# Performance work log

Hardware: AMD Instinct MI355X
Metric: run time of the kernel (lower is better)

Reference implementation:

```python
import jax, jax.numpy as jnp
import numpy as np


def setup_inputs() -> dict:
    key = jax.random.key(0)
    k1, k2 = jax.random.split(key)
    N, K, D = 32768, 1024, 512
    x = jax.random.normal(k1, (N, D), dtype=jnp.float32)
    centers = jax.random.normal(k2, (K, D), dtype=jnp.float32)
    return {"x": x, "centers": centers}


def reference(x, centers):
    # broadcasted (x[:,None]-c[None])**2 sum without the O(N*K*D) intermediate)
    x_sq = jnp.sum(x * x, axis=-1, keepdims=True)           # [N, 1]
    c_sq = jnp.sum(centers * centers, axis=-1)              # [K]
    cross = jnp.einsum('nd,kd->nk', x, centers)             # [N, K]
    norm_squared = x_sq + c_sq[None, :] - 2.0 * cross       # [N, K]
    # exp(-d/2) / sum_k exp(-d/2) == softmax(-d/2) over clusters
    probabilities = jax.nn.softmax(-0.5 * norm_squared, axis=1)
    return probabilities
```

## Files before the change

kernel.cpp:

```cpp
#include <hip/hip_runtime.h>
#include <stdint.h>


namespace {
constexpr int N_ROWS  = 32768;
constexpr int K_CL    = 1024;
constexpr int D_DIM   = 512;
constexpr int BM      = 64;
constexpr int THREADS = 512;
constexpr int WAVES   = 8;
constexpr int NSLICE  = 16;
}

typedef __bf16 bf16_t;
typedef __bf16 bf16x8 __attribute__((ext_vector_type(8)));
typedef __bf16 bf16x4 __attribute__((ext_vector_type(4)));
typedef float  f32x4  __attribute__((ext_vector_type(4)));

__global__ __launch_bounds__(64) void prep_kernel(const float* __restrict__ centers,
                                                  bf16_t* __restrict__ bpack,
                                                  float* __restrict__ bias) {
  const int col = blockIdx.x, lane = threadIdx.x;
  const int t = lane >> 2, g = lane & 3;
  const float* src = centers + (size_t)col * D_DIM + lane * 8;
  bf16x8 hi, lo;
  float ssq = 0.f;
  #pragma unroll
  for (int i = 0; i < 8; ++i) {
    float v = src[i];
    ssq += v * v;
    bf16_t h = (bf16_t)v;
    hi[i] = h;
    lo[i] = (bf16_t)(v - (float)h);
  }
  const int jh = col >> 9, c = col & 511;
  *(bf16x8*)(bpack + ((size_t)(4 * t + jh)     * 2048 + g * 512 + c) * 8) = hi;
  *(bf16x8*)(bpack + ((size_t)(4 * t + 2 + jh) * 2048 + g * 512 + c) * 8) = lo;
  for (int off = 32; off; off >>= 1) ssq += __shfl_down(ssq, off, 64);
  if (lane == 0) bias[col] = -0.5f * ssq;
}

__global__ __launch_bounds__(THREADS, 2) void cluster_kernel(
    const float* __restrict__ x, const bf16_t* __restrict__ bpack,
    const float* __restrict__ bias, float* __restrict__ out) {
  __shared__ bf16_t Abuf[2][2][2048];
  __shared__ float  red[WAVES * BM];
  __shared__ float  fin[BM];

  const int tid  = threadIdx.x;
  const int wid  = tid >> 6;
  const int lane = tid & 63;
  const int g    = lane >> 4;
  const int l15  = lane & 15;
  const int brow = blockIdx.x * BM;
  const int xrow = tid >> 3, q = tid & 7, gk = q >> 1, qh = q & 1;

  float bcol[8];
  #pragma unroll
  for (int cc = 0; cc < 8; ++cc)
    bcol[cc] = bias[(cc >> 2) * 512 + wid * 64 + (cc & 3) * 16 + l15];

  f32x4 acc[4][8];
  #pragma unroll
  for (int rb = 0; rb < 4; ++rb)
    #pragma unroll
    for (int cc = 0; cc < 8; ++cc) acc[rb][cc] = (f32x4){0.f, 0.f, 0.f, 0.f};

  const bf16x8* bbase =
      (const bf16x8*)bpack + ((size_t)g * 512 + wid * 64 + l15);

#define LOADB(S, DST)                                                          \
  {                                                                            \
    const bf16x8* p_ = bbase + (size_t)(S) * 2048;                             \
    _Pragma("unroll")                                                          \
    for (int cb_ = 0; cb_ < 4; ++cb_) (DST)[cb_] = p_[cb_ * 16];               \
  }
#define CONVERT(XV, PAR)                                                       \
  {                                                                            \
    bf16x4 h4_, l4_;                                                           \
    float vv_[4] = {(XV).x, (XV).y, (XV).z, (XV).w};                           \
    _Pragma("unroll")                                                          \
    for (int i_ = 0; i_ < 4; ++i_) {                                           \
      bf16_t h_ = (bf16_t)vv_[i_];                                             \
      h4_[i_] = h_;                                                            \
      l4_[i_] = (bf16_t)(vv_[i_] - (float)h_);                                 \
    }                                                                          \
    *(bf16x4*)&Abuf[(PAR)][0][(gk * 64 + xrow) * 8 + qh * 4] = h4_;            \
    *(bf16x4*)&Abuf[(PAR)][1][(gk * 64 + xrow) * 8 + qh * 4] = l4_;            \
  }
#define COMPUTE(BREG, HALF, WITH_LO)                                           \
  {                                                                            \
    _Pragma("unroll")                                                          \
    for (int cb = 0; cb < 4; ++cb) {                                           \
      _Pragma("unroll")                                                        \
      for (int rb = 0; rb < 4; ++rb)                                           \
        acc[rb][(HALF) * 4 + cb] = __builtin_amdgcn_mfma_f32_16x16x32_bf16(    \
            ahi[rb], (BREG)[cb], acc[rb][(HALF) * 4 + cb], 0, 0, 0);           \
      if (WITH_LO) {                                                           \
        _Pragma("unroll")                                                      \
        for (int rb = 0; rb < 4; ++rb)                                         \
          acc[rb][(HALF) * 4 + cb] = __builtin_amdgcn_mfma_f32_16x16x32_bf16(  \
              alo[rb], (BREG)[cb], acc[rb][(HALF) * 4 + cb], 0, 0, 0);         \
      }                                                                        \
    }                                                                          \
  }

  const float* xbase = x + (size_t)(brow + xrow) * D_DIM + q * 4;
  bf16x8 bcur[4], bnxt[4];

  {
    float4 xv0 = *(const float4*)xbase;
    CONVERT(xv0, 0)
    LOADB(0, bcur)
  }
  __syncthreads();

  bf16x8 ahi[4], alo[4];

  #pragma unroll 1
  for (int t = 0; t < NSLICE; ++t) {
    const int s0 = 4 * t;

    #pragma unroll
    for (int rb = 0; rb < 4; ++rb) {
      ahi[rb] = *(const bf16x8*)&Abuf[t & 1][0][(g * 64 + rb * 16 + l15) * 8];
      alo[rb] = *(const bf16x8*)&Abuf[t & 1][1][(g * 64 + rb * 16 + l15) * 8];
    }

    LOADB(s0 + 1, bnxt)
    COMPUTE(bcur, 0, 1)

    LOADB(s0 + 2, bcur)
    float4 xv = *(const float4*)(xbase + ((t + 1) & 15) * 32);
    COMPUTE(bnxt, 1, 1)

    LOADB(s0 + 3, bnxt)
    CONVERT(xv, (t + 1) & 1)
    COMPUTE(bcur, 0, 0)

    LOADB((s0 + 4) & 63, bcur)
    COMPUTE(bnxt, 1, 0)

    __syncthreads();
  }

  float rmax[4][4];
  #pragma unroll
  for (int rb = 0; rb < 4; ++rb) {
    #pragma unroll
    for (int j = 0; j < 4; ++j) {
      float m = -3.0e38f;
      #pragma unroll
      for (int cc = 0; cc < 8; ++cc) {
        float v = acc[rb][cc][j] + bcol[cc];
        acc[rb][cc][j] = v;
        m = fmaxf(m, v);
      }
      m = fmaxf(m, __shfl_xor(m, 1, 64));
      m = fmaxf(m, __shfl_xor(m, 2, 64));
      m = fmaxf(m, __shfl_xor(m, 4, 64));
      m = fmaxf(m, __shfl_xor(m, 8, 64));
      rmax[rb][j] = m;
    }
  }
  if (l15 == 0) {
    #pragma unroll
    for (int rb = 0; rb < 4; ++rb)
      #pragma unroll
      for (int j = 0; j < 4; ++j)
        red[wid * BM + rb * 16 + g * 4 + j] = rmax[rb][j];
  }
  __syncthreads();
  if (tid < BM) {
    float m = red[tid];
    #pragma unroll
    for (int w = 1; w < WAVES; ++w) m = fmaxf(m, red[w * BM + tid]);
    fin[tid] = m;
  }
  __syncthreads();

  #pragma unroll
  for (int rb = 0; rb < 4; ++rb) {
    #pragma unroll
    for (int j = 0; j < 4; ++j) {
      float m = fin[rb * 16 + g * 4 + j];
      float s = 0.f;
      #pragma unroll
      for (int cc = 0; cc < 8; ++cc) {
        float e = __expf(acc[rb][cc][j] - m);
        acc[rb][cc][j] = e;
        s += e;
      }
      s += __shfl_xor(s, 1, 64);
      s += __shfl_xor(s, 2, 64);
      s += __shfl_xor(s, 4, 64);
      s += __shfl_xor(s, 8, 64);
      rmax[rb][j] = s;
    }
  }
  __syncthreads();
  if (l15 == 0) {
    #pragma unroll
    for (int rb = 0; rb < 4; ++rb)
      #pragma unroll
      for (int j = 0; j < 4; ++j)
        red[wid * BM + rb * 16 + g * 4 + j] = rmax[rb][j];
  }
  __syncthreads();
  if (tid < BM) {
    float s = 0.f;
    #pragma unroll
    for (int w = 0; w < WAVES; ++w) s += red[w * BM + tid];
    fin[tid] = 1.0f / s;
  }
  __syncthreads();

  #pragma unroll
  for (int rb = 0; rb < 4; ++rb) {
    #pragma unroll
    for (int j = 0; j < 4; ++j) {
      const int row = rb * 16 + g * 4 + j;
      const float rs = fin[row];
      #pragma unroll
      for (int cc = 0; cc < 8; ++cc) {
        const int col = (cc >> 2) * 512 + wid * 64 + (cc & 3) * 16 + l15;
        out[(size_t)(brow + row) * K_CL + col] = acc[rb][cc][j] * rs;
      }
    }
  }
}

extern "C" void kernel_launch(void* const* d_in, const int* in_sizes, int n_in,
                              void* d_out, int out_size, void* d_ws, size_t ws_size,
                              hipStream_t stream) {
  const float* x       = (const float*)d_in[0];
  const float* centers = (const float*)d_in[1];
  float* out = (float*)d_out;

  bf16_t* bpack = (bf16_t*)d_ws;
  float*  bias  = (float*)((char*)d_ws + (size_t)64 * 32768);

  prep_kernel<<<K_CL, 64, 0, stream>>>(centers, bpack, bias);
  cluster_kernel<<<N_ROWS / BM, THREADS, 0, stream>>>(x, bpack, bias, out);
}
```

Baseline: 109.5 us.

## Stage B fragments through a 4-deep async global-to-LDS ring buffer

```diff
diff --git a/kernel.cpp b/kernel.cpp
--- a/kernel.cpp
+++ b/kernel.cpp
@@ -17,6 +17,12 @@
 typedef __bf16 bf16x4 __attribute__((ext_vector_type(4)));
 typedef float  f32x4  __attribute__((ext_vector_type(4)));
 
+__device__ inline void async_copy16(const void* g, void* l) {
+  __builtin_amdgcn_global_load_lds(
+      (const __attribute__((address_space(1))) uint32_t*)g,
+      (__attribute__((address_space(3))) uint32_t*)l, 16, 0, 0);
+}
+
 __global__ __launch_bounds__(64) void prep_kernel(const float* __restrict__ centers,
                                                   bf16_t* __restrict__ bpack,
                                                   float* __restrict__ bias) {
@@ -43,6 +49,7 @@
 __global__ __launch_bounds__(THREADS, 2) void cluster_kernel(
     const float* __restrict__ x, const bf16_t* __restrict__ bpack,
     const float* __restrict__ bias, float* __restrict__ out) {
+  __shared__ bf16_t Bbuf[4][16384];
   __shared__ bf16_t Abuf[2][2][2048];
   __shared__ float  red[WAVES * BM];
   __shared__ float  fin[BM];
@@ -55,25 +62,20 @@
   const int brow = blockIdx.x * BM;
   const int xrow = tid >> 3, q = tid & 7, gk = q >> 1, qh = q & 1;
 
-  float bcol[8];
-  #pragma unroll
-  for (int cc = 0; cc < 8; ++cc)
-    bcol[cc] = bias[(cc >> 2) * 512 + wid * 64 + (cc & 3) * 16 + l15];
-
   f32x4 acc[4][8];
   #pragma unroll
   for (int rb = 0; rb < 4; ++rb)
     #pragma unroll
     for (int cc = 0; cc < 8; ++cc) acc[rb][cc] = (f32x4){0.f, 0.f, 0.f, 0.f};
 
-  const bf16x8* bbase =
-      (const bf16x8*)bpack + ((size_t)g * 512 + wid * 64 + l15);
-
-#define LOADB(S, DST)                                                          \
+#define STAGE_B(S)                                                             \
   {                                                                            \
-    const bf16x8* p_ = bbase + (size_t)(S) * 2048;                             \
-    _Pragma("unroll")                                                          \
-    for (int cb_ = 0; cb_ < 4; ++cb_) (DST)[cb_] = p_[cb_ * 16];               \
+    const char* gs_ = (const char*)bpack + (size_t)((S) & 63) * 32768 +        \
+                      wid * 4096 + lane * 16;                                  \
+    char* ld_ = (char*)&Bbuf[(S) & 3][0] + wid * 4096;                         \
+    _Pragma("unroll")                                                          \
+    for (int i_ = 0; i_ < 4; ++i_)                                             \
+      async_copy16(gs_ + i_ * 1024, ld_ + i_ * 1024);                          \
   }
 #define CONVERT(XV, PAR)                                                       \
   {                                                                            \
@@ -88,32 +90,45 @@
     *(bf16x4*)&Abuf[(PAR)][0][(gk * 64 + xrow) * 8 + qh * 4] = h4_;            \
     *(bf16x4*)&Abuf[(PAR)][1][(gk * 64 + xrow) * 8 + qh * 4] = l4_;            \
   }
-#define COMPUTE(BREG, HALF, WITH_LO)                                           \
+#define COMPUTE(BUF, HALF, WITH_LO)                                            \
   {                                                                            \
+    const bf16_t* bb = &Bbuf[(BUF)][0];                                        \
+    bf16x8 bfrag[4];                                                           \
+    _Pragma("unroll")                                                          \
+    for (int cb = 0; cb < 4; ++cb)                                             \
+      bfrag[cb] = *(const bf16x8*)&bb[(g * 512 + wid * 64 + cb * 16 + l15) * 8]; \
+    __builtin_amdgcn_s_setprio(1);                                             \
     _Pragma("unroll")                                                          \
     for (int cb = 0; cb < 4; ++cb) {                                           \
       _Pragma("unroll")                                                        \
       for (int rb = 0; rb < 4; ++rb)                                           \
         acc[rb][(HALF) * 4 + cb] = __builtin_amdgcn_mfma_f32_16x16x32_bf16(    \
-            ahi[rb], (BREG)[cb], acc[rb][(HALF) * 4 + cb], 0, 0, 0);           \
+            ahi[rb], bfrag[cb], acc[rb][(HALF) * 4 + cb], 0, 0, 0);            \
       if (WITH_LO) {                                                           \
         _Pragma("unroll")                                                      \
         for (int rb = 0; rb < 4; ++rb)                                         \
           acc[rb][(HALF) * 4 + cb] = __builtin_amdgcn_mfma_f32_16x16x32_bf16(  \
-              alo[rb], (BREG)[cb], acc[rb][(HALF) * 4 + cb], 0, 0, 0);         \
+              alo[rb], bfrag[cb], acc[rb][(HALF) * 4 + cb], 0, 0, 0);          \
       }                                                                        \
     }                                                                          \
-  }
+    __builtin_amdgcn_s_setprio(0);                                             \
+  }
+#define FENCE(VMSTR)                                                           \
+    asm volatile(VMSTR ::: "memory");                                          \
+    __builtin_amdgcn_s_barrier();                                              \
+    __builtin_amdgcn_sched_barrier(0);
 
   const float* xbase = x + (size_t)(brow + xrow) * D_DIM + q * 4;
-  bf16x8 bcur[4], bnxt[4];
-
+
+  STAGE_B(0)
+  STAGE_B(1)
+  STAGE_B(2)
+  __builtin_amdgcn_sched_barrier(0);
   {
     float4 xv0 = *(const float4*)xbase;
     CONVERT(xv0, 0)
-    LOADB(0, bcur)
-  }
-  __syncthreads();
+  }
+  FENCE("s_waitcnt vmcnt(8) lgkmcnt(0)")
 
   bf16x8 ahi[4], alo[4];
 
@@ -121,28 +136,40 @@
   for (int t = 0; t < NSLICE; ++t) {
     const int s0 = 4 * t;
 
+    STAGE_B(s0 + 3)
+    __builtin_amdgcn_sched_barrier(0);
     #pragma unroll
     for (int rb = 0; rb < 4; ++rb) {
       ahi[rb] = *(const bf16x8*)&Abuf[t & 1][0][(g * 64 + rb * 16 + l15) * 8];
       alo[rb] = *(const bf16x8*)&Abuf[t & 1][1][(g * 64 + rb * 16 + l15) * 8];
     }
-
-    LOADB(s0 + 1, bnxt)
-    COMPUTE(bcur, 0, 1)
-
-    LOADB(s0 + 2, bcur)
+    COMPUTE(0, 0, 1)
+    FENCE("s_waitcnt vmcnt(8) lgkmcnt(0)")
+
     float4 xv = *(const float4*)(xbase + ((t + 1) & 15) * 32);
-    COMPUTE(bnxt, 1, 1)
-
-    LOADB(s0 + 3, bnxt)
+    STAGE_B(s0 + 4)
+    __builtin_amdgcn_sched_barrier(0);
+    COMPUTE(1, 1, 1)
+    FENCE("s_waitcnt vmcnt(9) lgkmcnt(0)")
+
     CONVERT(xv, (t + 1) & 1)
-    COMPUTE(bcur, 0, 0)
-
-    LOADB((s0 + 4) & 63, bcur)
-    COMPUTE(bnxt, 1, 0)
-
-    __syncthreads();
-  }
+    STAGE_B(s0 + 5)
+    __builtin_amdgcn_sched_barrier(0);
+    COMPUTE(2, 0, 0)
+    FENCE("s_waitcnt vmcnt(8) lgkmcnt(0)")
+
+    STAGE_B(s0 + 6)
+    __builtin_amdgcn_sched_barrier(0);
+    COMPUTE(3, 1, 0)
+    FENCE("s_waitcnt vmcnt(8) lgkmcnt(0)")
+  }
+
+  __syncthreads();
+
+  float bcol[8];
+  #pragma unroll
+  for (int cc = 0; cc < 8; ++cc)
+    bcol[cc] = bias[(cc >> 2) * 512 + wid * 64 + (cc & 3) * 16 + l15];
 
   float rmax[4][4];
   #pragma unroll
```

Result: slower. 152.4 us (+39.2%).

## Switch GEMM to fp16 32x32x16 MFMA and drop the x low-part split

Applied to the files above, without the earlier changes.

```diff
diff --git a/kernel.cpp b/kernel.cpp
--- a/kernel.cpp
+++ b/kernel.cpp
@@ -12,163 +12,160 @@
 constexpr int NSLICE  = 16;
 }
 
-typedef __bf16 bf16_t;
-typedef __bf16 bf16x8 __attribute__((ext_vector_type(8)));
-typedef __bf16 bf16x4 __attribute__((ext_vector_type(4)));
-typedef float  f32x4  __attribute__((ext_vector_type(4)));
+typedef _Float16 f16_t;
+typedef _Float16 f16x8 __attribute__((ext_vector_type(8)));
+typedef _Float16 f16x4 __attribute__((ext_vector_type(4)));
+typedef float    f32x16 __attribute__((ext_vector_type(16)));
 
 __global__ __launch_bounds__(64) void prep_kernel(const float* __restrict__ centers,
-                                                  bf16_t* __restrict__ bpack,
+                                                  f16_t* __restrict__ bpack,
                                                   float* __restrict__ bias) {
   const int col = blockIdx.x, lane = threadIdx.x;
-  const int t = lane >> 2, g = lane & 3;
+  const int t  = lane >> 2;
+  const int ks = (lane >> 1) & 1;
+  const int kh = lane & 1;
   const float* src = centers + (size_t)col * D_DIM + lane * 8;
-  bf16x8 hi, lo;
+  f16x8 hi, lo;
   float ssq = 0.f;
   #pragma unroll
   for (int i = 0; i < 8; ++i) {
     float v = src[i];
     ssq += v * v;
-    bf16_t h = (bf16_t)v;
+    f16_t h = (f16_t)v;
     hi[i] = h;
-    lo[i] = (bf16_t)(v - (float)h);
-  }
-  const int jh = col >> 9, c = col & 511;
-  *(bf16x8*)(bpack + ((size_t)(4 * t + jh)     * 2048 + g * 512 + c) * 8) = hi;
-  *(bf16x8*)(bpack + ((size_t)(4 * t + 2 + jh) * 2048 + g * 512 + c) * 8) = lo;
-  for (int off = 32; off; off >>= 1) ssq += __shfl_down(ssq, off, 64);
+    lo[i] = (f16_t)(v - (float)h);
+  }
+  const int jh = col >> 9, cb = (col & 511) >> 5, c32 = col & 31;
+  const size_t off = ((size_t)ks * 16 + cb) * 512 + (c32 * 2 + kh) * 8;
+  *(f16x8*)(bpack + (size_t)(4 * t + jh)     * 16384 + off) = hi;
+  *(f16x8*)(bpack + (size_t)(4 * t + 2 + jh) * 16384 + off) = lo;
+  for (int o = 32; o; o >>= 1) ssq += __shfl_down(ssq, o, 64);
   if (lane == 0) bias[col] = -0.5f * ssq;
 }
 
 __global__ __launch_bounds__(THREADS, 2) void cluster_kernel(
-    const float* __restrict__ x, const bf16_t* __restrict__ bpack,
+    const float* __restrict__ x, const f16_t* __restrict__ bpack,
     const float* __restrict__ bias, float* __restrict__ out) {
-  __shared__ bf16_t Abuf[2][2][2048];
-  __shared__ float  red[WAVES * BM];
-  __shared__ float  fin[BM];
+  __shared__ f16_t Abuf[2][4][64][8];
+  __shared__ float red[WAVES * BM];
+  __shared__ float fin[BM];
 
   const int tid  = threadIdx.x;
   const int wid  = tid >> 6;
   const int lane = tid & 63;
-  const int g    = lane >> 4;
-  const int l15  = lane & 15;
+  const int l31  = lane & 31;
+  const int h    = lane >> 5;
   const int brow = blockIdx.x * BM;
-  const int xrow = tid >> 3, q = tid & 7, gk = q >> 1, qh = q & 1;
-
-  float bcol[8];
-  #pragma unroll
-  for (int cc = 0; cc < 8; ++cc)
-    bcol[cc] = bias[(cc >> 2) * 512 + wid * 64 + (cc & 3) * 16 + l15];
-
-  f32x4 acc[4][8];
-  #pragma unroll
-  for (int rb = 0; rb < 4; ++rb)
-    #pragma unroll
-    for (int cc = 0; cc < 8; ++cc) acc[rb][cc] = (f32x4){0.f, 0.f, 0.f, 0.f};
-
-  const bf16x8* bbase =
-      (const bf16x8*)bpack + ((size_t)g * 512 + wid * 64 + l15);
+  const int xrow = tid >> 3, q8 = tid & 7;
+
+  f32x16 acc[2][4];
+  #pragma unroll
+  for (int rb = 0; rb < 2; ++rb)
+    #pragma unroll
+    for (int cc = 0; cc < 4; ++cc)
+      #pragma unroll
+      for (int e = 0; e < 16; ++e) acc[rb][cc][e] = 0.f;
+
+  const char* bbase = (const char*)bpack + wid * 2048 + (l31 * 2 + h) * 16;
+  const float* xbase = x + (size_t)(brow + xrow) * D_DIM + q8 * 4;
 
 #define LOADB(S, DST)                                                          \
   {                                                                            \
-    const bf16x8* p_ = bbase + (size_t)(S) * 2048;                             \
-    _Pragma("unroll")                                                          \
-    for (int cb_ = 0; cb_ < 4; ++cb_) (DST)[cb_] = p_[cb_ * 16];               \
+    const char* p_ = bbase + (size_t)((S) & 63) * 32768;                       \
+    (DST)[0] = *(const f16x8*)(p_);                          \
+    (DST)[1] = *(const f16x8*)(p_ + 1024);                   \
+    (DST)[2] = *(const f16x8*)(p_ + 16384);                  \
+    (DST)[3] = *(const f16x8*)(p_ + 17408);                  \
   }
 #define CONVERT(XV, PAR)                                                       \
   {                                                                            \
-    bf16x4 h4_, l4_;                                                           \
-    float vv_[4] = {(XV).x, (XV).y, (XV).z, (XV).w};                           \
-    _Pragma("unroll")                                                          \
-    for (int i_ = 0; i_ < 4; ++i_) {                                           \
-      bf16_t h_ = (bf16_t)vv_[i_];                                             \
-      h4_[i_] = h_;                                                            \
-      l4_[i_] = (bf16_t)(vv_[i_] - (float)h_);                                 \
-    }                                                                          \
-    *(bf16x4*)&Abuf[(PAR)][0][(gk * 64 + xrow) * 8 + qh * 4] = h4_;            \
-    *(bf16x4*)&Abuf[(PAR)][1][(gk * 64 + xrow) * 8 + qh * 4] = l4_;            \
-  }
-#define COMPUTE(BREG, HALF, WITH_LO)                                           \
+    f16x4 h4_;                                                                 \
+    h4_[0] = (f16_t)(XV).x; h4_[1] = (f16_t)(XV).y;                            \
+    h4_[2] = (f16_t)(XV).z; h4_[3] = (f16_t)(XV).w;                            \
+    *(f16x4*)&Abuf[(PAR)][q8 >> 1][xrow][(q8 & 1) * 4] = h4_;                  \
+  }
+#define COMPUTE(B, JH)                                                         \
   {                                                                            \
     _Pragma("unroll")                                                          \
-    for (int cb = 0; cb < 4; ++cb) {                                           \
+    for (int ks_ = 0; ks_ < 2; ++ks_)                                          \
       _Pragma("unroll")                                                        \
-      for (int rb = 0; rb < 4; ++rb)                                           \
-        acc[rb][(HALF) * 4 + cb] = __builtin_amdgcn_mfma_f32_16x16x32_bf16(    \
-            ahi[rb], (BREG)[cb], acc[rb][(HALF) * 4 + cb], 0, 0, 0);           \
-      if (WITH_LO) {                                                           \
+      for (int c2_ = 0; c2_ < 2; ++c2_) {                                      \
         _Pragma("unroll")                                                      \
-        for (int rb = 0; rb < 4; ++rb)                                         \
-          acc[rb][(HALF) * 4 + cb] = __builtin_amdgcn_mfma_f32_16x16x32_bf16(  \
-              alo[rb], (BREG)[cb], acc[rb][(HALF) * 4 + cb], 0, 0, 0);         \
+        for (int rb_ = 0; rb_ < 2; ++rb_)                                      \
+          acc[rb_][(JH) * 2 + c2_] = __builtin_amdgcn_mfma_f32_32x32x16_f16(   \
+              a[rb_][ks_], (B)[ks_ * 2 + c2_], acc[rb_][(JH) * 2 + c2_],       \
+              0, 0, 0);                                                        \
       }                                                                        \
-    }                                                                          \
-  }
-
-  const float* xbase = x + (size_t)(brow + xrow) * D_DIM + q * 4;
-  bf16x8 bcur[4], bnxt[4];
+  }
+
+  f16x8 bcur[4], bnxt[4];
 
   {
     float4 xv0 = *(const float4*)xbase;
     CONVERT(xv0, 0)
-    LOADB(0, bcur)
-  }
-  __syncthreads();
-
-  bf16x8 ahi[4], alo[4];
+  }
+  LOADB(0, bcur)
+  __syncthreads();
+
+  f16x8 a[2][2];
 
   #pragma unroll 1
   for (int t = 0; t < NSLICE; ++t) {
+    #pragma unroll
+    for (int rb = 0; rb < 2; ++rb)
+      #pragma unroll
+      for (int ks = 0; ks < 2; ++ks)
+        a[rb][ks] = *(const f16x8*)&Abuf[t & 1][ks * 2 + h][rb * 32 + l31][0];
+
     const int s0 = 4 * t;
 
-    #pragma unroll
-    for (int rb = 0; rb < 4; ++rb) {
-      ahi[rb] = *(const bf16x8*)&Abuf[t & 1][0][(g * 64 + rb * 16 + l15) * 8];
-      alo[rb] = *(const bf16x8*)&Abuf[t & 1][1][(g * 64 + rb * 16 + l15) * 8];
-    }
-
     LOADB(s0 + 1, bnxt)
-    COMPUTE(bcur, 0, 1)
+    float4 xv = *(const float4*)(xbase + ((t + 1) & 15) * 32);
+    COMPUTE(bcur, 0)
 
     LOADB(s0 + 2, bcur)
-    float4 xv = *(const float4*)(xbase + ((t + 1) & 15) * 32);
-    COMPUTE(bnxt, 1, 1)
+    COMPUTE(bnxt, 1)
 
     LOADB(s0 + 3, bnxt)
     CONVERT(xv, (t + 1) & 1)
-    COMPUTE(bcur, 0, 0)
+    COMPUTE(bcur, 0)
 
     LOADB((s0 + 4) & 63, bcur)
-    COMPUTE(bnxt, 1, 0)
+    COMPUTE(bnxt, 1)
 
     __syncthreads();
   }
 
-  float rmax[4][4];
-  #pragma unroll
-  for (int rb = 0; rb < 4; ++rb) {
-    #pragma unroll
-    for (int j = 0; j < 4; ++j) {
+  float bcol[4];
+  #pragma unroll
+  for (int cc = 0; cc < 4; ++cc)
+    bcol[cc] = bias[(cc >> 1) * 512 + wid * 64 + (cc & 1) * 32 + l31];
+
+  float rr[2][16];
+  #pragma unroll
+  for (int rb = 0; rb < 2; ++rb)
+    #pragma unroll
+    for (int reg = 0; reg < 16; ++reg) {
       float m = -3.0e38f;
       #pragma unroll
-      for (int cc = 0; cc < 8; ++cc) {
-        float v = acc[rb][cc][j] + bcol[cc];
-        acc[rb][cc][j] = v;
+      for (int cc = 0; cc < 4; ++cc) {
+        float v = acc[rb][cc][reg] + bcol[cc];
+        acc[rb][cc][reg] = v;
         m = fmaxf(m, v);
       }
       m = fmaxf(m, __shfl_xor(m, 1, 64));
       m = fmaxf(m, __shfl_xor(m, 2, 64));
       m = fmaxf(m, __shfl_xor(m, 4, 64));
       m = fmaxf(m, __shfl_xor(m, 8, 64));
-      rmax[rb][j] = m;
+      m = fmaxf(m, __shfl_xor(m, 16, 64));
+      rr[rb][reg] = m;
     }
-  }
-  if (l15 == 0) {
-    #pragma unroll
-    for (int rb = 0; rb < 4; ++rb)
-      #pragma unroll
-      for (int j = 0; j < 4; ++j)
-        red[wid * BM + rb * 16 + g * 4 + j] = rmax[rb][j];
+  if (l31 == 0) {
+    #pragma unroll
+    for (int rb = 0; rb < 2; ++rb)
+      #pragma unroll
+      for (int reg = 0; reg < 16; ++reg)
+        red[wid * BM + rb * 32 + (reg & 3) + 8 * (reg >> 2) + 4 * h] = rr[rb][reg];
   }
   __syncthreads();
   if (tid < BM) {
@@ -180,31 +177,31 @@
   __syncthreads();
 
   #pragma unroll
-  for (int rb = 0; rb < 4; ++rb) {
-    #pragma unroll
-    for (int j = 0; j < 4; ++j) {
-      float m = fin[rb * 16 + g * 4 + j];
+  for (int rb = 0; rb < 2; ++rb)
+    #pragma unroll
+    for (int reg = 0; reg < 16; ++reg) {
+      const float m = fin[rb * 32 + (reg & 3) + 8 * (reg >> 2) + 4 * h];
       float s = 0.f;
       #pragma unroll
-      for (int cc = 0; cc < 8; ++cc) {
-        float e = __expf(acc[rb][cc][j] - m);
-        acc[rb][cc][j] = e;
+      for (int cc = 0; cc < 4; ++cc) {
+        float e = __expf(acc[rb][cc][reg] - m);
+        acc[rb][cc][reg] = e;
         s += e;
       }
       s += __shfl_xor(s, 1, 64);
       s += __shfl_xor(s, 2, 64);
       s += __shfl_xor(s, 4, 64);
       s += __shfl_xor(s, 8, 64);
-      rmax[rb][j] = s;
+      s += __shfl_xor(s, 16, 64);
+      rr[rb][reg] = s;
     }
-  }
-  __syncthreads();
-  if (l15 == 0) {
-    #pragma unroll
-    for (int rb = 0; rb < 4; ++rb)
-      #pragma unroll
-      for (int j = 0; j < 4; ++j)
-        red[wid * BM + rb * 16 + g * 4 + j] = rmax[rb][j];
+  __syncthreads();
+  if (l31 == 0) {
+    #pragma unroll
+    for (int rb = 0; rb < 2; ++rb)
+      #pragma unroll
+      for (int reg = 0; reg < 16; ++reg)
+        red[wid * BM + rb * 32 + (reg & 3) + 8 * (reg >> 2) + 4 * h] = rr[rb][reg];
   }
   __syncthreads();
   if (tid < BM) {
@@ -216,18 +213,17 @@
   __syncthreads();
 
   #pragma unroll
-  for (int rb = 0; rb < 4; ++rb) {
-    #pragma unroll
-    for (int j = 0; j < 4; ++j) {
-      const int row = rb * 16 + g * 4 + j;
+  for (int rb = 0; rb < 2; ++rb)
+    #pragma unroll
+    for (int reg = 0; reg < 16; ++reg) {
+      const int row = rb * 32 + (reg & 3) + 8 * (reg >> 2) + 4 * h;
       const float rs = fin[row];
       #pragma unroll
-      for (int cc = 0; cc < 8; ++cc) {
-        const int col = (cc >> 2) * 512 + wid * 64 + (cc & 3) * 16 + l15;
-        out[(size_t)(brow + row) * K_CL + col] = acc[rb][cc][j] * rs;
+      for (int cc = 0; cc < 4; ++cc) {
+        const int col = (cc >> 1) * 512 + wid * 64 + (cc & 1) * 32 + l31;
+        out[(size_t)(brow + row) * K_CL + col] = acc[rb][cc][reg] * rs;
       }
     }
-  }
 }
 
 extern "C" void kernel_launch(void* const* d_in, const int* in_sizes, int n_in,
@@ -237,8 +233,8 @@
   const float* centers = (const float*)d_in[1];
   float* out = (float*)d_out;
 
-  bf16_t* bpack = (bf16_t*)d_ws;
-  float*  bias  = (float*)((char*)d_ws + (size_t)64 * 32768);
+  f16_t* bpack = (f16_t*)d_ws;
+  float* bias  = (float*)((char*)d_ws + (size_t)64 * 32768);
 
   prep_kernel<<<K_CL, 64, 0, stream>>>(centers, bpack, bias);
   cluster_kernel<<<N_ROWS / BM, THREADS, 0, stream>>>(x, bpack, bias, out);
```

Measured after the change: 123.4 us. 12.6% more time.
